# Performance work log

Measured on AMD Instinct MI355X. Metric: run time of the kernel, lower is better.

The kernel has to match this reference:

```python
import jax, jax.numpy as jnp
import numpy as np

EMBED_DIM = 768
NUM_HEADS = 12
HEAD_DIM = EMBED_DIM // NUM_HEADS
SCALE = HEAD_DIM ** -0.5


def setup_inputs() -> dict:
    key = jax.random.key(0)
    k1, k2, k3, k4, k5 = jax.random.split(key, 5)
    B, T = 8, 1024
    hidden_states = jax.random.normal(k1, (B, T, EMBED_DIM), dtype=jnp.float32)
    init = 0.02
    qkv_w = jax.random.normal(k2, (EMBED_DIM, 3 * EMBED_DIM), dtype=jnp.float32) * init
    qkv_b = jnp.zeros((3 * EMBED_DIM,), dtype=jnp.float32)
    proj_w = jax.random.normal(k3, (EMBED_DIM, EMBED_DIM), dtype=jnp.float32) * init
    proj_b = jnp.zeros((EMBED_DIM,), dtype=jnp.float32)
    return {
        "hidden_states": hidden_states,
        "qkv_w": qkv_w,
        "qkv_b": qkv_b,
        "proj_w": proj_w,
        "proj_b": proj_b,
    }


def reference(hidden_states, qkv_w, qkv_b, proj_w, proj_b):
    B, T, C = hidden_states.shape
    # fused QKV projection
    mixed = hidden_states @ qkv_w + qkv_b            # [B, T, 3C]
    mixed = mixed.reshape(B, T, 3, NUM_HEADS, HEAD_DIM)
    mixed = jnp.transpose(mixed, (2, 0, 3, 1, 4))    # [3, B, H, T, D]
    q, k, v = mixed[0], mixed[1], mixed[2]
    # scaled dot-product attention (dropout is identity in eval)
    scores = jnp.einsum("bhqd,bhkd->bhqk", q, k) * SCALE
    probs = jax.nn.softmax(scores, axis=-1)
    ctx = jnp.einsum("bhqk,bhkd->bhqd", probs, v)    # [B, H, T, D]
    ctx = jnp.transpose(ctx, (0, 2, 1, 3)).reshape(B, T, C)
    out = ctx @ proj_w + proj_b
    return out
```

## Files before the change

### kernel.cpp

```cpp
#include <hip/hip_runtime.h>

#define EMBED 768
#define NHEAD 12
#define HDIM 64
#define BATCH 8
#define SEQ 1024
#define ROWS (BATCH*SEQ)
#define QKVN (3*EMBED)
#define ATTN_SCALE 0.125f

typedef short s16x8 __attribute__((ext_vector_type(8)));
typedef short s16x4 __attribute__((ext_vector_type(4)));
typedef float f32x4 __attribute__((ext_vector_type(4)));

__device__ __forceinline__ float bf2f(unsigned short u) {
    union { unsigned int i; float f; } v; v.i = ((unsigned int)u) << 16; return v.f;
}
__device__ __forceinline__ unsigned short f2bf(float f) {
    unsigned int i = __builtin_bit_cast(unsigned int, f);
    i += 0x7FFFu + ((i >> 16) & 1u);
    return (unsigned short)(i >> 16);
}

__device__ __forceinline__ void async16(short* lds, const unsigned short* g) {
    __builtin_amdgcn_global_load_lds(
        (const __attribute__((address_space(1))) unsigned int*)g,
        (__attribute__((address_space(3))) unsigned int*)lds,
        16, 0, 0);
}

__device__ __forceinline__ f32x4 mfma16(s16x4 a, s16x4 b, f32x4 c) {
#if __has_builtin(__builtin_amdgcn_mfma_f32_16x16x16bf16_1k)
    return __builtin_amdgcn_mfma_f32_16x16x16bf16_1k(a, b, c, 0, 0, 0);
#else
    asm volatile("v_mfma_f32_16x16x16_bf16 %0, %1, %2, %0" : "+v"(c) : "v"(a), "v"(b));
    return c;
#endif
}

__global__ __launch_bounds__(256) void prep_k(
    const float* __restrict__ qkv_w, unsigned short* __restrict__ WqkvT,
    const float* __restrict__ proj_w, unsigned short* __restrict__ WprojT,
    const float* __restrict__ hidden, unsigned short* __restrict__ hiddenBf)
{
    __shared__ float tile[64][65];
    int blk = blockIdx.x;
    int t = threadIdx.x;
    if (blk < 576) {
        const float* in; unsigned short* outp; int K, N, tx, ty;
        if (blk < 432) { in = qkv_w; outp = WqkvT; K = EMBED; N = QKVN; tx = blk % 36; ty = blk / 36; }
        else { int b2 = blk - 432; in = proj_w; outp = WprojT; K = EMBED; N = EMBED; tx = b2 % 12; ty = b2 / 12; }
        int n0 = tx * 64, k0 = ty * 64;
        int c = t & 63, r0 = t >> 6;
        #pragma unroll
        for (int i = 0; i < 16; i++) {
            int r = r0 * 16 + i;
            tile[r][c] = in[(long long)(k0 + r) * N + n0 + c];
        }
        __syncthreads();
        #pragma unroll
        for (int i = 0; i < 16; i++) {
            int nr = r0 * 16 + i;
            outp[(long long)(n0 + nr) * K + k0 + c] = f2bf(tile[c][nr]);
        }
    } else {
        int tid = (blk - 576) * 256 + t;
        int base = tid * 8;
        float4 f0 = *(const float4*)&hidden[base];
        float4 f1 = *(const float4*)&hidden[base + 4];
        s16x8 a;
        a[0] = (short)f2bf(f0.x); a[1] = (short)f2bf(f0.y);
        a[2] = (short)f2bf(f0.z); a[3] = (short)f2bf(f0.w);
        a[4] = (short)f2bf(f1.x); a[5] = (short)f2bf(f1.y);
        a[6] = (short)f2bf(f1.z); a[7] = (short)f2bf(f1.w);
        *(s16x8*)&hiddenBf[base] = a;
    }
}

template <int OUT_F32, int BN>
__global__ __launch_bounds__(256) void gemm128(
    const unsigned short* __restrict__ A,
    const unsigned short* __restrict__ Bt,
    const float* __restrict__ bias,
    void* __restrict__ Cv,
    int M, int N, int K)
{
    constexpr int WN = (BN == 128) ? 64 : 32;
    constexpr int NJ = WN / 16;
    __shared__ short As[2][128 * 32];
    __shared__ short Bs[2][BN * 32];
    int t = threadIdx.x, lane = t & 63, w = t >> 6;
    int quad = lane >> 4, low = lane & 15;
    int orig = blockIdx.y * gridDim.x + blockIdx.x;
    int xcd = orig & 7;
    int local = orig >> 3;
    int bx = xcd * 8 + (local & 7);
    int by = local >> 3;
    int m0 = bx * 128, n0 = by * BN;
    int wm = (w & 1) * 64, wn = (w >> 1) * WN;

    int ci0 = w * 128 + lane;
    int r0 = ci0 >> 2, c0 = (ci0 & 3) ^ ((r0 >> 1) & 3);
    int ci1 = ci0 + 64;
    int r1 = ci1 >> 2, c1 = (ci1 & 3) ^ ((r1 >> 1) & 3);
    const unsigned short* pa0 = A + (long long)(m0 + r0) * K + c0 * 8;
    const unsigned short* pa1 = A + (long long)(m0 + r1) * K + c1 * 8;
    int alo0 = (w * 128) * 8;
    int alo1 = (w * 128 + 64) * 8;
    int cib0 = (BN == 128) ? (w * 128 + lane) : (w * 64 + lane);
    int rb0 = cib0 >> 2, cb0 = (cib0 & 3) ^ ((rb0 >> 1) & 3);
    const unsigned short* pb0 = Bt + (long long)(n0 + rb0) * K + cb0 * 8;
    int blo0 = (BN == 128) ? (w * 128) * 8 : (w * 64) * 8;
    int cib1 = cib0 + 64;
    int rb1 = cib1 >> 2, cb1 = (cib1 & 3) ^ ((rb1 >> 1) & 3);
    const unsigned short* pb1 = Bt + (long long)(n0 + rb1) * K + cb1 * 8;
    int blo1 = (w * 128 + 64) * 8;

    async16(&As[0][alo0], pa0);
    async16(&As[0][alo1], pa1);
    async16(&Bs[0][blo0], pb0);
    if (BN == 128) async16(&Bs[0][blo1], pb1);
    __syncthreads();

    f32x4 acc[4][NJ] = {};
    int cur = 0;
    for (int k0 = 0; k0 < K; k0 += 32) {
        int nxt = cur ^ 1;
        if (k0 + 32 < K) {
            async16(&As[nxt][alo0], pa0 + k0 + 32);
            async16(&As[nxt][alo1], pa1 + k0 + 32);
            async16(&Bs[nxt][blo0], pb0 + k0 + 32);
            if (BN == 128) async16(&Bs[nxt][blo1], pb1 + k0 + 32);
        }
        const short* as = As[cur];
        const short* bs = Bs[cur];
        s16x8 af[4], bfr[NJ];
        #pragma unroll
        for (int i = 0; i < 4; i++) {
            int ra = wm + i * 16 + low;
            af[i] = *(const s16x8*)&as[ra * 32 + ((quad ^ ((ra >> 1) & 3)) * 8)];
        }
        #pragma unroll
        for (int j = 0; j < NJ; j++) {
            int rbn = wn + j * 16 + low;
            bfr[j] = *(const s16x8*)&bs[rbn * 32 + ((quad ^ ((rbn >> 1) & 3)) * 8)];
        }
        #pragma unroll
        for (int i = 0; i < 4; i++)
            #pragma unroll
            for (int j = 0; j < NJ; j++)
                acc[i][j] = __builtin_amdgcn_mfma_f32_16x16x32_bf16(af[i], bfr[j], acc[i][j], 0, 0, 0);
        __syncthreads();
        cur = nxt;
    }
    #pragma unroll
    for (int i = 0; i < 4; i++)
        #pragma unroll
        for (int j = 0; j < NJ; j++)
            #pragma unroll
            for (int r = 0; r < 4; r++) {
                int m = m0 + wm + i * 16 + quad * 4 + r;
                int n = n0 + wn + j * 16 + low;
                float v = acc[i][j][r] + bias[n];
                if (OUT_F32) ((float*)Cv)[(long long)m * N + n] = v;
                else ((unsigned short*)Cv)[(long long)m * N + n] = f2bf(v);
            }
}

__global__ __launch_bounds__(512) void attn_k(
    const unsigned short* __restrict__ mixed,
    unsigned short* __restrict__ ctx)
{
    __shared__ __align__(16) char smem[34816];
    int blk = blockIdx.x;
    int bh = blk % 96;
    int qc = blk / 96;
    int b = bh / NHEAD, h = bh - b * NHEAD;
    int t = threadIdx.x;
    int tl = t & 255;
    int lane = t & 63, w = t >> 6;
    int wq = w & 3, gang = w >> 2;
    int quad = lane >> 4, low = lane & 15;
    long long rowbase = (long long)b * SEQ;
    int q0 = qc * 128 + wq * 32;
    int hoff = h * HDIM;

    short* Ks = (short*)(smem + gang * 16896);
    short* Vt = (short*)(smem + gang * 16896 + 8192);

    s16x8 qf[2][2];
    #pragma unroll
    for (int qh = 0; qh < 2; qh++) {
        long long r = (rowbase + q0 + qh * 16 + low) * QKVN + hoff;
        qf[qh][0] = *(const s16x8*)&mixed[r + quad * 8];
        qf[qh][1] = *(const s16x8*)&mixed[r + 32 + quad * 8];
    }

    int s0 = wq * 128 + lane;
    int kr0 = s0 >> 3, kc0 = s0 & 7;
    int kg = kc0 ^ (kr0 & 7);
    const unsigned short* pk0 = mixed + (rowbase + kr0) * QKVN + EMBED + hoff + kg * 8;
    const unsigned short* pk1 = mixed + (rowbase + kr0 + 8) * QKVN + EMBED + hoff + kg * 8;
    short* lk0 = Ks + (wq * 128) * 8;
    short* lk1 = Ks + (wq * 128 + 64) * 8;

    int dblk = tl & 15, rq = tl >> 4;
    const unsigned short* pv = mixed + (rowbase + rq * 4) * QKVN + 2 * EMBED + hoff + dblk * 4;

    f32x4 o[2][4] = {};
    float lsum[2] = {0.f, 0.f};

    int kvbase = gang * 512;
    for (int it = 0; it < 8; it++) {
        long long koff = (long long)(kvbase + it * 64) * QKVN;
        __syncthreads();
        async16(lk0, pk0 + koff);
        async16(lk1, pk1 + koff);
        s16x4 v0 = *(const s16x4*)&pv[koff];
        s16x4 v1 = *(const s16x4*)&pv[koff + QKVN];
        s16x4 v2 = *(const s16x4*)&pv[koff + 2 * QKVN];
        s16x4 v3 = *(const s16x4*)&pv[koff + 3 * QKVN];
        #pragma unroll
        for (int k = 0; k < 4; k++) {
            s16x4 wv;
            wv[0] = v0[k]; wv[1] = v1[k]; wv[2] = v2[k]; wv[3] = v3[k];
            *(s16x4*)&Vt[(dblk * 4 + k) * 68 + rq * 4] = wv;
        }
        __syncthreads();

        f32x4 sT[2][4] = {};
        __builtin_amdgcn_s_setprio(1);
        #pragma unroll
        for (int n = 0; n < 4; n++) {
            int rr = n * 16 + low;
            int key = low & 7;
            s16x8 kf0 = *(const s16x8*)&Ks[rr * 64 + ((quad ^ key) * 8)];
            s16x8 kf1 = *(const s16x8*)&Ks[rr * 64 + (((quad + 4) ^ key) * 8)];
            sT[0][n] = __builtin_amdgcn_mfma_f32_16x16x32_bf16(kf0, qf[0][0], sT[0][n], 0, 0, 0);
            sT[0][n] = __builtin_amdgcn_mfma_f32_16x16x32_bf16(kf1, qf[0][1], sT[0][n], 0, 0, 0);
            sT[1][n] = __builtin_amdgcn_mfma_f32_16x16x32_bf16(kf0, qf[1][0], sT[1][n], 0, 0, 0);
            sT[1][n] = __builtin_amdgcn_mfma_f32_16x16x32_bf16(kf1, qf[1][1], sT[1][n], 0, 0, 0);
        }
        __builtin_amdgcn_s_setprio(0);

        s16x4 pf[2][4];
        #pragma unroll
        for (int qh = 0; qh < 2; qh++)
            #pragma unroll
            for (int n = 0; n < 4; n++) {
                float e0 = __expf(sT[qh][n][0] * ATTN_SCALE);
                float e1 = __expf(sT[qh][n][1] * ATTN_SCALE);
                float e2 = __expf(sT[qh][n][2] * ATTN_SCALE);
                float e3 = __expf(sT[qh][n][3] * ATTN_SCALE);
                lsum[qh] += (e0 + e1) + (e2 + e3);
                unsigned int w0, w1;
                asm("v_cvt_pk_bf16_f32 %0, %1, %2" : "=v"(w0) : "v"(e0), "v"(e1));
                asm("v_cvt_pk_bf16_f32 %0, %1, %2" : "=v"(w1) : "v"(e2), "v"(e3));
                union { unsigned int u[2]; s16x4 v; } pu;
                pu.u[0] = w0; pu.u[1] = w1;
                pf[qh][n] = pu.v;
            }

        __builtin_amdgcn_s_setprio(1);
        #pragma unroll
        for (int nt = 0; nt < 4; nt++) {
            int drow = nt * 16 + low;
            #pragma unroll
            for (int n = 0; n < 4; n++) {
                s16x4 vf = *(const s16x4*)&Vt[drow * 68 + n * 16 + quad * 4];
                o[0][nt] = mfma16(pf[0][n], vf, o[0][nt]);
                o[1][nt] = mfma16(pf[1][n], vf, o[1][nt]);
            }
        }
        __builtin_amdgcn_s_setprio(0);
    }

    #pragma unroll
    for (int qh = 0; qh < 2; qh++) {
        lsum[qh] += __shfl_xor(lsum[qh], 16, 64);
        lsum[qh] += __shfl_xor(lsum[qh], 32, 64);
    }

    f32x4* xo = (f32x4*)smem;
    float*  xl = (float*)(smem + 32768);
    __syncthreads();
    if (gang == 1) {
        #pragma unroll
        for (int qh = 0; qh < 2; qh++) {
            #pragma unroll
            for (int nt = 0; nt < 4; nt++)
                xo[((wq * 2 + qh) * 4 + nt) * 64 + lane] = o[qh][nt];
            xl[(wq * 2 + qh) * 64 + lane] = lsum[qh];
        }
    }
    __syncthreads();
    if (gang == 0) {
        #pragma unroll
        for (int qh = 0; qh < 2; qh++) {
            #pragma unroll
            for (int nt = 0; nt < 4; nt++)
                o[qh][nt] += xo[((wq * 2 + qh) * 4 + nt) * 64 + lane];
            lsum[qh] += xl[(wq * 2 + qh) * 64 + lane];
        }
        #pragma unroll
        for (int qh = 0; qh < 2; qh++)
            #pragma unroll
            for (int r = 0; r < 4; r++) {
                float inv = 1.0f / __shfl(lsum[qh], quad * 4 + r, 64);
                int q = q0 + qh * 16 + quad * 4 + r;
                #pragma unroll
                for (int nt = 0; nt < 4; nt++)
                    ctx[(rowbase + q) * EMBED + hoff + nt * 16 + low] =
                        f2bf(o[qh][nt][r] * inv);
            }
    }
}

extern "C" void kernel_launch(void* const* d_in, const int* in_sizes, int n_in,
                              void* d_out, int out_size, void* d_ws, size_t ws_size,
                              hipStream_t stream) {
    const float* hidden = (const float*)d_in[0];
    const float* qkv_w  = (const float*)d_in[1];
    const float* qkv_b  = (const float*)d_in[2];
    const float* proj_w = (const float*)d_in[3];
    const float* proj_b = (const float*)d_in[4];
    float* out = (float*)d_out;

    char* ws = (char*)d_ws;
    unsigned short* hiddenBf = (unsigned short*)ws;
    unsigned short* ctx      = (unsigned short*)ws;
    unsigned short* WqkvT    = (unsigned short*)(ws + 12582912);
    unsigned short* WprojT   = (unsigned short*)(ws + 16121856);
    unsigned short* mixed    = (unsigned short*)(ws + 17301504);

    prep_k<<<dim3(3648), 256, 0, stream>>>(qkv_w, WqkvT, proj_w, WprojT, hidden, hiddenBf);
    gemm128<0, 128><<<dim3(ROWS / 128, QKVN / 128), 256, 0, stream>>>(
        hiddenBf, WqkvT, qkv_b, mixed, ROWS, QKVN, EMBED);
    attn_k<<<dim3(96 * 8), 512, 0, stream>>>(mixed, ctx);
    gemm128<1, 64><<<dim3(ROWS / 128, EMBED / 64), 256, 0, stream>>>(
        ctx, WprojT, proj_b, out, ROWS, EMBED, EMBED);
}
```

Measured before the change: 189.9 us.

## Fuse hidden-state fp32-to-bf16 conversion into the QKV GEMM A-tile loads

Removes the separate pass that converted hidden states to bf16 in the prep kernel. The QKV GEMM now reads fp32 A rows directly into registers, converts them with packed bf16 conversion instructions, and writes them to swizzled LDS after the MFMA block. This removes a full write and re-read of the bf16 hidden buffer and shrinks the prep launch. In exchange the A path no longer uses async direct-to-LDS loads. It reads twice as many bytes per tile, and prefetch now depends on registers and explicit LDS stores.

```diff
diff --git a/kernel.cpp b/kernel.cpp
--- a/kernel.cpp
+++ b/kernel.cpp
@@ -38,48 +38,45 @@
 #endif
 }
 
+__device__ __forceinline__ s16x8 cvt8(float4 a, float4 b) {
+    unsigned int w0, w1, w2, w3;
+    asm("v_cvt_pk_bf16_f32 %0, %1, %2" : "=v"(w0) : "v"(a.x), "v"(a.y));
+    asm("v_cvt_pk_bf16_f32 %0, %1, %2" : "=v"(w1) : "v"(a.z), "v"(a.w));
+    asm("v_cvt_pk_bf16_f32 %0, %1, %2" : "=v"(w2) : "v"(b.x), "v"(b.y));
+    asm("v_cvt_pk_bf16_f32 %0, %1, %2" : "=v"(w3) : "v"(b.z), "v"(b.w));
+    union { unsigned int u[4]; s16x8 v; } r;
+    r.u[0] = w0; r.u[1] = w1; r.u[2] = w2; r.u[3] = w3;
+    return r.v;
+}
+
 __global__ __launch_bounds__(256) void prep_k(
     const float* __restrict__ qkv_w, unsigned short* __restrict__ WqkvT,
-    const float* __restrict__ proj_w, unsigned short* __restrict__ WprojT,
-    const float* __restrict__ hidden, unsigned short* __restrict__ hiddenBf)
+    const float* __restrict__ proj_w, unsigned short* __restrict__ WprojT)
 {
     __shared__ float tile[64][65];
     int blk = blockIdx.x;
     int t = threadIdx.x;
-    if (blk < 576) {
-        const float* in; unsigned short* outp; int K, N, tx, ty;
-        if (blk < 432) { in = qkv_w; outp = WqkvT; K = EMBED; N = QKVN; tx = blk % 36; ty = blk / 36; }
-        else { int b2 = blk - 432; in = proj_w; outp = WprojT; K = EMBED; N = EMBED; tx = b2 % 12; ty = b2 / 12; }
-        int n0 = tx * 64, k0 = ty * 64;
-        int c = t & 63, r0 = t >> 6;
-        #pragma unroll
-        for (int i = 0; i < 16; i++) {
-            int r = r0 * 16 + i;
-            tile[r][c] = in[(long long)(k0 + r) * N + n0 + c];
-        }
-        __syncthreads();
-        #pragma unroll
-        for (int i = 0; i < 16; i++) {
-            int nr = r0 * 16 + i;
-            outp[(long long)(n0 + nr) * K + k0 + c] = f2bf(tile[c][nr]);
-        }
-    } else {
-        int tid = (blk - 576) * 256 + t;
-        int base = tid * 8;
-        float4 f0 = *(const float4*)&hidden[base];
-        float4 f1 = *(const float4*)&hidden[base + 4];
-        s16x8 a;
-        a[0] = (short)f2bf(f0.x); a[1] = (short)f2bf(f0.y);
-        a[2] = (short)f2bf(f0.z); a[3] = (short)f2bf(f0.w);
-        a[4] = (short)f2bf(f1.x); a[5] = (short)f2bf(f1.y);
-        a[6] = (short)f2bf(f1.z); a[7] = (short)f2bf(f1.w);
-        *(s16x8*)&hiddenBf[base] = a;
-    }
-}
-
-template <int OUT_F32, int BN>
+    const float* in; unsigned short* outp; int K, N, tx, ty;
+    if (blk < 432) { in = qkv_w; outp = WqkvT; K = EMBED; N = QKVN; tx = blk % 36; ty = blk / 36; }
+    else { int b2 = blk - 432; in = proj_w; outp = WprojT; K = EMBED; N = EMBED; tx = b2 % 12; ty = b2 / 12; }
+    int n0 = tx * 64, k0 = ty * 64;
+    int c = t & 63, r0 = t >> 6;
+    #pragma unroll
+    for (int i = 0; i < 16; i++) {
+        int r = r0 * 16 + i;
+        tile[r][c] = in[(long long)(k0 + r) * N + n0 + c];
+    }
+    __syncthreads();
+    #pragma unroll
+    for (int i = 0; i < 16; i++) {
+        int nr = r0 * 16 + i;
+        outp[(long long)(n0 + nr) * K + k0 + c] = f2bf(tile[c][nr]);
+    }
+}
+
+template <int OUT_F32, int BN, int A_F32>
 __global__ __launch_bounds__(256) void gemm128(
-    const unsigned short* __restrict__ A,
+    const void* __restrict__ Av,
     const unsigned short* __restrict__ Bt,
     const float* __restrict__ bias,
     void* __restrict__ Cv,
@@ -103,10 +100,19 @@
     int r0 = ci0 >> 2, c0 = (ci0 & 3) ^ ((r0 >> 1) & 3);
     int ci1 = ci0 + 64;
     int r1 = ci1 >> 2, c1 = (ci1 & 3) ^ ((r1 >> 1) & 3);
-    const unsigned short* pa0 = A + (long long)(m0 + r0) * K + c0 * 8;
-    const unsigned short* pa1 = A + (long long)(m0 + r1) * K + c1 * 8;
-    int alo0 = (w * 128) * 8;
-    int alo1 = (w * 128 + 64) * 8;
+    const unsigned short* pa0 = nullptr; const unsigned short* pa1 = nullptr;
+    const float* fa0 = nullptr; const float* fa1 = nullptr;
+    if constexpr (A_F32) {
+        fa0 = (const float*)Av + (long long)(m0 + r0) * K + c0 * 8;
+        fa1 = (const float*)Av + (long long)(m0 + r1) * K + c1 * 8;
+    } else {
+        pa0 = (const unsigned short*)Av + (long long)(m0 + r0) * K + c0 * 8;
+        pa1 = (const unsigned short*)Av + (long long)(m0 + r1) * K + c1 * 8;
+    }
+    int alo0 = ci0 * 8;
+    int alo1 = ci1 * 8;
+    int awlo0 = (w * 128) * 8;
+    int awlo1 = (w * 128 + 64) * 8;
     int cib0 = (BN == 128) ? (w * 128 + lane) : (w * 64 + lane);
     int rb0 = cib0 >> 2, cb0 = (cib0 & 3) ^ ((rb0 >> 1) & 3);
     const unsigned short* pb0 = Bt + (long long)(n0 + rb0) * K + cb0 * 8;
@@ -116,8 +122,17 @@
     const unsigned short* pb1 = Bt + (long long)(n0 + rb1) * K + cb1 * 8;
     int blo1 = (w * 128 + 64) * 8;
 
-    async16(&As[0][alo0], pa0);
-    async16(&As[0][alo1], pa1);
+    if constexpr (A_F32) {
+        float4 a0 = *(const float4*)&fa0[0];
+        float4 a1 = *(const float4*)&fa0[4];
+        float4 a2 = *(const float4*)&fa1[0];
+        float4 a3 = *(const float4*)&fa1[4];
+        *(s16x8*)&As[0][alo0] = cvt8(a0, a1);
+        *(s16x8*)&As[0][alo1] = cvt8(a2, a3);
+    } else {
+        async16(&As[0][awlo0], pa0);
+        async16(&As[0][awlo1], pa1);
+    }
     async16(&Bs[0][blo0], pb0);
     if (BN == 128) async16(&Bs[0][blo1], pb1);
     __syncthreads();
@@ -126,9 +141,18 @@
     int cur = 0;
     for (int k0 = 0; k0 < K; k0 += 32) {
         int nxt = cur ^ 1;
-        if (k0 + 32 < K) {
-            async16(&As[nxt][alo0], pa0 + k0 + 32);
-            async16(&As[nxt][alo1], pa1 + k0 + 32);
+        bool pf = (k0 + 32 < K);
+        float4 na0, na1, na2, na3;
+        if (pf) {
+            if constexpr (A_F32) {
+                na0 = *(const float4*)&fa0[k0 + 32];
+                na1 = *(const float4*)&fa0[k0 + 36];
+                na2 = *(const float4*)&fa1[k0 + 32];
+                na3 = *(const float4*)&fa1[k0 + 36];
+            } else {
+                async16(&As[nxt][awlo0], pa0 + k0 + 32);
+                async16(&As[nxt][awlo1], pa1 + k0 + 32);
+            }
             async16(&Bs[nxt][blo0], pb0 + k0 + 32);
             if (BN == 128) async16(&Bs[nxt][blo1], pb1 + k0 + 32);
         }
@@ -150,6 +174,12 @@
             #pragma unroll
             for (int j = 0; j < NJ; j++)
                 acc[i][j] = __builtin_amdgcn_mfma_f32_16x16x32_bf16(af[i], bfr[j], acc[i][j], 0, 0, 0);
+        if (pf) {
+            if constexpr (A_F32) {
+                *(s16x8*)&As[nxt][alo0] = cvt8(na0, na1);
+                *(s16x8*)&As[nxt][alo1] = cvt8(na2, na3);
+            }
+        }
         __syncthreads();
         cur = nxt;
     }
@@ -327,16 +357,15 @@
     float* out = (float*)d_out;
 
     char* ws = (char*)d_ws;
-    unsigned short* hiddenBf = (unsigned short*)ws;
     unsigned short* ctx      = (unsigned short*)ws;
     unsigned short* WqkvT    = (unsigned short*)(ws + 12582912);
     unsigned short* WprojT   = (unsigned short*)(ws + 16121856);
     unsigned short* mixed    = (unsigned short*)(ws + 17301504);
 
-    prep_k<<<dim3(3648), 256, 0, stream>>>(qkv_w, WqkvT, proj_w, WprojT, hidden, hiddenBf);
-    gemm128<0, 128><<<dim3(ROWS / 128, QKVN / 128), 256, 0, stream>>>(
-        hiddenBf, WqkvT, qkv_b, mixed, ROWS, QKVN, EMBED);
+    prep_k<<<dim3(576), 256, 0, stream>>>(qkv_w, WqkvT, proj_w, WprojT);
+    gemm128<0, 128, 1><<<dim3(ROWS / 128, QKVN / 128), 256, 0, stream>>>(
+        hidden, WqkvT, qkv_b, mixed, ROWS, QKVN, EMBED);
     attn_k<<<dim3(96 * 8), 512, 0, stream>>>(mixed, ctx);
-    gemm128<1, 64><<<dim3(ROWS / 128, EMBED / 64), 256, 0, stream>>>(
+    gemm128<1, 64, 0><<<dim3(ROWS / 128, EMBED / 64), 256, 0, stream>>>(
         ctx, WprojT, proj_b, out, ROWS, EMBED, EMBED);
 }
```

Measured after the change: 192.8 us. About the same (+1.5%).
